# Optimization experiments

Measured on AMD Instinct MI355X. Metric: run time of the kernel, lower is better.

## Reference

```python
import jax, jax.numpy as jnp
import numpy as np
from jax.scipy.linalg import solve_triangular

REG = 1e-6  # reg_covar added to covariance diagonal
LOG2PI = float(np.log(2.0 * np.pi))
RESP_EPS = 10.0 * float(np.finfo(np.float32).eps)


def _log_gauss(X, means, covs):
    # X: [N,D], means: [K,D], covs: [K,D,D] -> per-sample per-component log N(x|mu_k, Sigma_k): [N,K]
    K, D = means.shape
    eye = jnp.eye(D, dtype=X.dtype)
    chol = jnp.linalg.cholesky(covs + REG * eye)                      # [K,D,D]
    diff = X[None, :, :] - means[:, None, :]                          # [K,N,D]
    sol = jax.vmap(lambda L, d: solve_triangular(L, d.T, lower=True))(chol, diff)  # [K,D,N]
    maha = jnp.sum(sol * sol, axis=1)                                 # [K,N]
    logdet = jnp.sum(jnp.log(jnp.diagonal(chol, axis1=1, axis2=2)), axis=1)  # [K] = 0.5*log|Sigma|
    return (-0.5 * (D * LOG2PI + maha) - logdet[:, None]).T           # [N,K]


def _em_step(X, weights, means, covs):
    N, D = X.shape
    # E-step: responsibilities via stable logsumexp
    lp = _log_gauss(X, means, covs) + jnp.log(weights)[None, :]       # [N,K]
    log_norm = jax.scipy.special.logsumexp(lp, axis=1)                # [N]
    resp = jnp.exp(lp - log_norm[:, None])                            # [N,K]
    # M-step (MLE)
    nk = resp.sum(axis=0) + RESP_EPS                                  # [K]
    new_w = nk / N
    new_means = (resp.T @ X) / nk[:, None]                            # [K,D]
    diff = X[None, :, :] - new_means[:, None, :]                      # [K,N,D]
    new_covs = jnp.einsum('kn,knd,kne->kde', resp.T, diff, diff) / nk[:, None, None]
    new_covs = new_covs + REG * jnp.eye(D, dtype=X.dtype)
    return new_w, new_means, new_covs


def reference(X, weights, means, covariances, n_iter):
    # Normalize provided weights (uniform init in the torch module)
    w0 = weights / jnp.sum(weights)

    def step(carry, _):
        w, m, c = carry
        return _em_step(X, w, m, c), None

    (w, m, c), _ = jax.lax.scan(step, (w0, means, covariances), xs=None, length=n_iter)
    # Final per-sample log-likelihood under the fitted mixture (lower bound)
    lp = _log_gauss(X, m, c) + jnp.log(w)[None, :]
    return jax.scipy.special.logsumexp(lp, axis=1)                    # [N]


def setup_inputs() -> dict:
    key = jax.random.key(0)
    kx, km = jax.random.split(key)
    N, D, K = 100000, 32, 16
    X = jax.random.normal(kx, (N, D), dtype=jnp.float32)
    weights = jnp.ones((K,), dtype=jnp.float32) / K
    means = jax.random.normal(km, (K, D), dtype=jnp.float32)
    covariances = jnp.tile(jnp.eye(D, dtype=jnp.float32)[None], (K, 1, 1))
    return {"X": X, "weights": weights, "means": means, "covariances": covariances, "n_iter": 5}
```

## Files before the change

kernel.cpp:

```cpp
#include <hip/hip_runtime.h>
#include <math.h>

#define REGC 1e-6f
#define LOG2PI 1.83787706640934534f
#define RESP_EPS 1.1920929e-6f

#define NPART_MAX 256
#define PART_K 1156
#define PART_BLK (16 * PART_K)
#define RS 16

typedef __attribute__((ext_vector_type(8))) short short8;
typedef __attribute__((ext_vector_type(4))) float f32x4;
typedef unsigned short ushort_t;
typedef unsigned int uint_t;

__device__ __forceinline__ ushort_t f2bf(float x) {
    uint_t u = __float_as_uint(x);
    uint_t r = (u + 0x7fffu + ((u >> 16) & 1u)) >> 16;
    return (ushort_t)r;
}
__device__ __forceinline__ float bf2f(ushort_t h) {
    return __uint_as_float(((uint_t)h) << 16);
}
__device__ __forceinline__ f32x4 shx4(f32x4 v, int m) {
    f32x4 r;
#pragma unroll
    for (int i = 0; i < 4; ++i) r[i] = __shfl_xor(v[i], m);
    return r;
}
__device__ __forceinline__ f32x4 sel4(bool s, f32x4 b, f32x4 a) {
    f32x4 r;
#pragma unroll
    for (int i = 0; i < 4; ++i) r[i] = s ? b[i] : a[i];
    return r;
}

__global__ void gmm_init(const float* __restrict__ w, const float* __restrict__ mu,
                         const float* __restrict__ cov, float* __restrict__ P0) {
    int t = blockIdx.x * 256 + threadIdx.x;
    if (t < 16) {
        float s = 0.f;
        for (int i = 0; i < 16; ++i) s += w[i];
        P0[t] = w[t] / s;
    } else if (t < 528) {
        P0[t] = mu[t - 16];
    } else if (t < 16912) {
        P0[t] = cov[t - 528];
    }
}

__global__ __launch_bounds__(256) void gmm_xsplit(const float* __restrict__ X,
                                                  ushort_t* __restrict__ Xh,
                                                  ushort_t* __restrict__ Xl,
                                                  ushort_t* __restrict__ XTH,
                                                  int N) {
    int chunk = blockIdx.x;
    int t = threadIdx.x;
    __shared__ float xsh[32][33];
    int s = t >> 3, q = t & 7;
    int n = chunk * 32 + s;
    float4 v = make_float4(0.f, 0.f, 0.f, 0.f);
    if (n < N) v = ((const float4*)(X + (size_t)n * 32))[q];
    float vv[4] = { v.x, v.y, v.z, v.w };
    xsh[s][q * 4 + 0] = v.x; xsh[s][q * 4 + 1] = v.y;
    xsh[s][q * 4 + 2] = v.z; xsh[s][q * 4 + 3] = v.w;
    if (n < N) {
        ushort_t h[4], l[4];
#pragma unroll
        for (int i = 0; i < 4; ++i) {
            h[i] = f2bf(vv[i]);
            l[i] = f2bf(vv[i] - bf2f(h[i]));
        }
        size_t o = (size_t)n * 32 + q * 4;
        uint2 hp = make_uint2((uint_t)h[0] | ((uint_t)h[1] << 16),
                              (uint_t)h[2] | ((uint_t)h[3] << 16));
        uint2 lp = make_uint2((uint_t)l[0] | ((uint_t)l[1] << 16),
                              (uint_t)l[2] | ((uint_t)l[3] << 16));
        *(uint2*)(Xh + o) = hp;
        *(uint2*)(Xl + o) = lp;
    }
    __syncthreads();
    int di = t >> 7;
    int lane = (t >> 1) & 63;
    int jj0 = (t & 1) * 4;
    int c = lane & 15, quad = lane >> 4;
    int d = di * 16 + c;
    ushort_t fh[4];
#pragma unroll
    for (int i = 0; i < 4; ++i) fh[i] = f2bf(xsh[quad * 8 + jj0 + i][d]);
    size_t fo = ((size_t)(chunk * 2 + di) * 64 + lane) * 8 + jj0;
    uint2 hp = make_uint2((uint_t)fh[0] | ((uint_t)fh[1] << 16),
                          (uint_t)fh[2] | ((uint_t)fh[3] << 16));
    *(uint2*)(XTH + fo) = hp;
}

__global__ __launch_bounds__(64) void gmm_prep(const float* __restrict__ P,
                                               ushort_t* __restrict__ Wh,
                                               ushort_t* __restrict__ Wl,
                                               float* __restrict__ Bv,
                                               float* __restrict__ Cc) {
    int k = blockIdx.x;
    int t = threadIdx.x;
    __shared__ float L[32][33];
    __shared__ float Ai[32][33];
    const float* cov = P + 528 + k * 1024;
    const float* mu  = P + 16 + k * 32;

#pragma unroll
    for (int rep = 0; rep < 16; ++rep) {
        int idx = rep * 64 + t;
        int i = idx >> 5, j = idx & 31;
        L[i][j] = cov[idx] + (i == j ? REGC : 0.f);
    }
    __syncthreads();

#pragma unroll
    for (int j = 0; j < 32; ++j) {
        float s = L[j][j];
#pragma unroll
        for (int p = 0; p < j; ++p) { float v = L[j][p]; s -= v * v; }
        float dj = sqrtf(s);
        if (t > j && t < 32) {
            float s2 = L[t][j];
#pragma unroll
            for (int p = 0; p < j; ++p) s2 -= L[t][p] * L[j][p];
            L[t][j] = s2 / dj;
        }
        if (t == j) L[j][j] = dj;
        __syncthreads();
    }

    if (t < 32) {
        float ai[32];
#pragma unroll
        for (int r = 0; r < 32; ++r) {
            float s = (r == t) ? 1.f : 0.f;
#pragma unroll
            for (int p = 0; p < r; ++p) s -= L[r][p] * ai[p];
            ai[r] = s / L[r][r];
        }
#pragma unroll
        for (int r = 0; r < 32; ++r) Ai[r][t] = ai[r];
    }
    __syncthreads();

#pragma unroll
    for (int rep = 0; rep < 16; ++rep) {
        int idx = rep * 64 + t;
        int i = idx >> 5, j = idx & 31;
        float v = Ai[i][j];
        ushort_t h = f2bf(v);
        Wh[(size_t)(k * 32 + i) * 32 + j] = h;
        Wl[(size_t)(k * 32 + i) * 32 + j] = f2bf(v - bf2f(h));
    }
    if (t < 32) {
        float s = 0.f;
#pragma unroll
        for (int j = 0; j < 32; ++j) s += Ai[t][j] * mu[j];
        Bv[k * 32 + t] = s;
    }
    float lv = (t < 32) ? logf(L[t & 31][t & 31]) : 0.f;
#pragma unroll
    for (int off = 1; off < 32; off <<= 1) lv += __shfl_xor(lv, off);
    if (t == 0) Cc[k] = logf(P[k]) - 0.5f * 32.0f * LOG2PI - lv;
}

__global__ __launch_bounds__(256, 2) void gmm_estep(const ushort_t* __restrict__ Xh,
                                                    const ushort_t* __restrict__ Xl,
                                                    const ushort_t* __restrict__ Wh,
                                                    const ushort_t* __restrict__ Wl,
                                                    const float* __restrict__ Bv,
                                                    const float* __restrict__ Cc,
                                                    float* __restrict__ resp,
                                                    float* __restrict__ out,
                                                    int N, int mode) {
    int t = threadIdx.x;
    int wave = t >> 6, lane = t & 63;
    int quad = lane >> 4, c = lane & 15;
    int wstart = (blockIdx.x * 4 + wave) * 32;
    if (wstart + 32 > N) wstart = (N >= 32) ? (N - 32) : 0;
    bool al4 = ((N & 3) == 0);

    size_t xo0 = (size_t)(wstart + c) * 32 + quad * 8;
    size_t xo1 = (size_t)(wstart + 16 + c) * 32 + quad * 8;
    short8 ah0 = *(const short8*)(Xh + xo0);
    short8 al0 = *(const short8*)(Xl + xo0);
    short8 ah1 = *(const short8*)(Xh + xo1);
    short8 al1 = *(const short8*)(Xl + xo1);

    f32x4 p0[2], p1[2], p2[2], p3[2], fin[2];

#pragma unroll
    for (int k = 0; k < 16; ++k) {
        size_t w0 = (size_t)(k * 32 + c) * 32 + quad * 8;
        size_t w1 = w0 + 512;
        short8 bh0 = *(const short8*)(Wh + w0);
        short8 bl0 = *(const short8*)(Wl + w0);
        short8 bh1 = *(const short8*)(Wh + w1);
        short8 bl1 = *(const short8*)(Wl + w1);
        float bv0 = Bv[k * 32 + c];
        float bv1 = Bv[k * 32 + 16 + c];
#pragma unroll
        for (int tt = 0; tt < 2; ++tt) {
            short8 ah = tt ? ah1 : ah0;
            short8 al = tt ? al1 : al0;
            f32x4 a0 = {0.f, 0.f, 0.f, 0.f};
            f32x4 a1 = {0.f, 0.f, 0.f, 0.f};
            a0 = __builtin_amdgcn_mfma_f32_16x16x32_bf16(ah, bh0, a0, 0, 0, 0);
            a0 = __builtin_amdgcn_mfma_f32_16x16x32_bf16(ah, bl0, a0, 0, 0, 0);
            a0 = __builtin_amdgcn_mfma_f32_16x16x32_bf16(al, bh0, a0, 0, 0, 0);
            a1 = __builtin_amdgcn_mfma_f32_16x16x32_bf16(ah, bh1, a1, 0, 0, 0);
            a1 = __builtin_amdgcn_mfma_f32_16x16x32_bf16(ah, bl1, a1, 0, 0, 0);
            a1 = __builtin_amdgcn_mfma_f32_16x16x32_bf16(al, bh1, a1, 0, 0, 0);
            f32x4 ms;
#pragma unroll
            for (int r = 0; r < 4; ++r) {
                float d0 = a0[r] - bv0;
                float d1 = a1[r] - bv1;
                ms[r] = fmaf(d0, d0, d1 * d1);
            }
            if ((k & 1) == 0) { p0[tt] = ms; }
            else {
                f32x4 a = p0[tt] + shx4(p0[tt], 1);
                f32x4 b = ms + shx4(ms, 1);
                f32x4 v = sel4((c & 1) != 0, b, a);
                if ((k & 2) == 0) { p1[tt] = v; }
                else {
                    a = p1[tt] + shx4(p1[tt], 2); b = v + shx4(v, 2); v = sel4((c & 2) != 0, b, a);
                    if ((k & 4) == 0) { p2[tt] = v; }
                    else {
                        a = p2[tt] + shx4(p2[tt], 4); b = v + shx4(v, 4); v = sel4((c & 4) != 0, b, a);
                        if ((k & 8) == 0) { p3[tt] = v; }
                        else {
                            a = p3[tt] + shx4(p3[tt], 8); b = v + shx4(v, 8);
                            fin[tt] = sel4((c & 8) != 0, b, a);
                        }
                    }
                }
            }
        }
    }

    float cc = Cc[c];
#pragma unroll
    for (int tt = 0; tt < 2; ++tt) {
        f32x4 lp;
#pragma unroll
        for (int r = 0; r < 4; ++r) lp[r] = cc - 0.5f * fin[tt][r];
        f32x4 mx = lp;
#pragma unroll
        for (int off = 1; off < 16; off <<= 1) {
            f32x4 s = shx4(mx, off);
#pragma unroll
            for (int r = 0; r < 4; ++r) mx[r] = fmaxf(mx[r], s[r]);
        }
        f32x4 e;
#pragma unroll
        for (int r = 0; r < 4; ++r) e[r] = __expf(lp[r] - mx[r]);
        f32x4 sm = e;
#pragma unroll
        for (int off = 1; off < 16; off <<= 1) sm = sm + shx4(sm, off);

        int nb = wstart + tt * 16 + quad * 4;
        if (mode) {
            if (c == 0) {
                f32x4 o;
#pragma unroll
                for (int r = 0; r < 4; ++r) o[r] = mx[r] + __logf(sm[r]);
                if (al4) *(f32x4*)(out + nb) = o;
                else { for (int r = 0; r < 4; ++r) out[nb + r] = o[r]; }
            }
        } else {
            f32x4 sv;
#pragma unroll
            for (int r = 0; r < 4; ++r) sv[r] = e[r] / sm[r];
            size_t off = (size_t)c * N + nb;
            if (al4) *(f32x4*)(resp + off) = sv;
            else { for (int r = 0; r < 4; ++r) resp[off + r] = sv[r]; }
        }
    }
}

__global__ __launch_bounds__(1024, 4) void gmm_moment(const ushort_t* __restrict__ XTH,
                                                      const float* __restrict__ resp,
                                                      float* __restrict__ part,
                                                      int N, int NC) {
    int t = threadIdx.x;
    int k = t >> 6;
    int lane = t & 63;
    int quad = lane >> 4, c = lane & 15;
    bool al4 = ((N & 3) == 0);

    f32x4 acc00 = {0.f,0.f,0.f,0.f}, acc01 = {0.f,0.f,0.f,0.f};
    f32x4 acc10 = {0.f,0.f,0.f,0.f}, acc11 = {0.f,0.f,0.f,0.f};
    float row0 = 0.f, row1 = 0.f, corner = 0.f;

#pragma unroll 1
    for (int chunk = blockIdx.x; chunk < NC; chunk += gridDim.x) {
        size_t fb = ((size_t)chunk * 2 * 64 + lane) * 8;
        short8 bh0 = *(const short8*)(XTH + fb);
        short8 bh1 = *(const short8*)(XTH + fb + 512);

        const float* rp = resp + (size_t)k * N + (size_t)chunk * 32 + quad * 8;
        float r[8];
        if (al4) {
            float4 ra = *(const float4*)rp;
            float4 rb = *(const float4*)(rp + 4);
            r[0]=ra.x; r[1]=ra.y; r[2]=ra.z; r[3]=ra.w;
            r[4]=rb.x; r[5]=rb.y; r[6]=rb.z; r[7]=rb.w;
        } else {
#pragma unroll
            for (int j = 0; j < 8; ++j) r[j] = rp[j];
        }
        corner += ((r[0]+r[1])+(r[2]+r[3])) + ((r[4]+r[5])+(r[6]+r[7]));

        short8 a0, a1;
#pragma unroll
        for (int jj = 0; jj < 8; ++jj) {
            float x0 = bf2f((ushort_t)bh0[jj]);
            float av0 = r[jj] * x0;
            a0[jj] = (short)f2bf(av0);
            row0 += av0;
            float x1 = bf2f((ushort_t)bh1[jj]);
            float av1 = r[jj] * x1;
            a1[jj] = (short)f2bf(av1);
            row1 += av1;
        }

        acc00 = __builtin_amdgcn_mfma_f32_16x16x32_bf16(a0, bh0, acc00, 0, 0, 0);
        acc01 = __builtin_amdgcn_mfma_f32_16x16x32_bf16(a0, bh1, acc01, 0, 0, 0);
        acc10 = __builtin_amdgcn_mfma_f32_16x16x32_bf16(a1, bh0, acc10, 0, 0, 0);
        acc11 = __builtin_amdgcn_mfma_f32_16x16x32_bf16(a1, bh1, acc11, 0, 0, 0);
    }

    row0 += __shfl_xor(row0, 16);  row0 += __shfl_xor(row0, 32);
    row1 += __shfl_xor(row1, 16);  row1 += __shfl_xor(row1, 32);
    corner += __shfl_xor(corner, 16);  corner += __shfl_xor(corner, 32);

    float* pb = part + ((size_t)blockIdx.x * 16 + k) * PART_K;
#pragma unroll
    for (int r = 0; r < 4; ++r) {
        pb[(quad * 4 + r) * 34 + c]            = acc00[r];
        pb[(quad * 4 + r) * 34 + 16 + c]       = acc01[r];
        pb[(16 + quad * 4 + r) * 34 + c]       = acc10[r];
        pb[(16 + quad * 4 + r) * 34 + 16 + c]  = acc11[r];
    }
    if (quad == 0) {
        pb[32 * 34 + c]      = row0;
        pb[32 * 34 + 16 + c] = row1;
    }
    if (lane == 0) pb[32 * 34 + 32] = corner;
}

__global__ __launch_bounds__(256) void gmm_reduce1(const float* __restrict__ part,
                                                   float* __restrict__ part2,
                                                   int npart) {
    int k = blockIdx.x, g = blockIdx.y;
    int nb = (npart + RS - 1) / RS;
    int b0 = g * nb;
    int b1 = b0 + nb; if (b1 > npart) b1 = npart;
    for (int idx = threadIdx.x; idx < PART_K; idx += 256) {
        float s = 0.f;
#pragma unroll 4
        for (int b = b0; b < b1; ++b)
            s += part[((size_t)b * 16 + k) * PART_K + idx];
        part2[((size_t)g * 16 + k) * PART_K + idx] = s;
    }
}

__global__ __launch_bounds__(256) void gmm_redfin_prep(const float* __restrict__ part2,
                                                       ushort_t* __restrict__ Wh,
                                                       ushort_t* __restrict__ Wl,
                                                       float* __restrict__ Bv,
                                                       float* __restrict__ Cc,
                                                       int N) {
    int k = blockIdx.x;
    int t = threadIdx.x;
    __shared__ float S[1156];
    __shared__ float L[32][33];
    __shared__ float Ai[32][33];

    for (int idx = t; idx < 1156; idx += 256) {
        float s = 0.f;
#pragma unroll
        for (int b = 0; b < RS; ++b)
            s += part2[((size_t)b * 16 + k) * PART_K + idx];
        S[idx] = s;
    }
    __syncthreads();
    float nk = S[32 * 34 + 32] + RESP_EPS;
    float inv = 1.f / nk;
    for (int idx = t; idx < 1024; idx += 256) {
        int i = idx >> 5, j = idx & 31;
        float mi = S[32 * 34 + i] * inv;
        float mj = S[32 * 34 + j] * inv;
        L[i][j] = S[i * 34 + j] * inv - mi * mj + ((i == j) ? 2.f * REGC : 0.f);
    }
    __syncthreads();

#pragma unroll
    for (int j = 0; j < 32; ++j) {
        if (t < 32) {
            float s = L[j][j];
#pragma unroll
            for (int p = 0; p < j; ++p) { float v = L[j][p]; s -= v * v; }
            float dj = sqrtf(s);
            if (t > j) {
                float s2 = L[t][j];
#pragma unroll
                for (int p = 0; p < j; ++p) s2 -= L[t][p] * L[j][p];
                L[t][j] = s2 / dj;
            }
            if (t == j) L[j][j] = dj;
        }
        __syncthreads();
    }

    if (t < 32) {
        float ai[32];
#pragma unroll
        for (int r = 0; r < 32; ++r) {
            float s = (r == t) ? 1.f : 0.f;
#pragma unroll
            for (int p = 0; p < r; ++p) s -= L[r][p] * ai[p];
            ai[r] = s / L[r][r];
        }
#pragma unroll
        for (int r = 0; r < 32; ++r) Ai[r][t] = ai[r];
    }
    __syncthreads();

#pragma unroll
    for (int rep = 0; rep < 4; ++rep) {
        int idx = rep * 256 + t;
        int i = idx >> 5, j = idx & 31;
        float v = Ai[i][j];
        ushort_t h = f2bf(v);
        Wh[(size_t)(k * 32 + i) * 32 + j] = h;
        Wl[(size_t)(k * 32 + i) * 32 + j] = f2bf(v - bf2f(h));
    }
    if (t < 32) {
        float s = 0.f;
#pragma unroll
        for (int j = 0; j < 32; ++j) s += Ai[t][j] * (S[32 * 34 + j] * inv);
        Bv[k * 32 + t] = s;
    }
    float lv = (t < 32) ? logf(L[t & 31][t & 31]) : 0.f;
#pragma unroll
    for (int off = 1; off < 32; off <<= 1) lv += __shfl_xor(lv, off);
    if (t == 0) Cc[k] = logf(nk / (float)N) - 0.5f * 32.0f * LOG2PI - lv;
}

extern "C" void kernel_launch(void* const* d_in, const int* in_sizes, int n_in,
                              void* d_out, int out_size, void* d_ws, size_t ws_size,
                              hipStream_t stream) {
    const float* X   = (const float*)d_in[0];
    const float* w   = (const float*)d_in[1];
    const float* mu  = (const float*)d_in[2];
    const float* cov = (const float*)d_in[3];
    const int NITER = 5;
    int N = in_sizes[0] / 32;
    int NC = (N + 31) / 32;

    float* ws = (float*)d_ws;
    float*    P0 = ws;
    float*    Bv = ws + 16912;
    float*    Cc = ws + 17424;
    ushort_t* Wh = (ushort_t*)(ws + 17440);
    ushort_t* Wl = (ushort_t*)(ws + 25632);
    ushort_t* Xh = (ushort_t*)(ws + 33824);
    ushort_t* Xl = (ushort_t*)(ws + 33824 + (size_t)16 * N);
    size_t xt0 = 33824 + (size_t)32 * N;
    size_t SZ  = (size_t)NC * 512;
    ushort_t* XTH = (ushort_t*)(ws + xt0);
    float*  resp = ws + xt0 + SZ;
    size_t p2base = xt0 + SZ + (size_t)16 * N;
    float*  part2 = ws + p2base;
    size_t pbase = p2base + (size_t)RS * 16 * PART_K;
    float*  part = ws + pbase;

    long long avail = (long long)(ws_size / 4) - (long long)pbase;
    int npart = (int)(avail / PART_BLK);
    if (npart > NPART_MAX) npart = NPART_MAX;
    if (npart < 1) npart = 1;

    float* out = (float*)d_out;

    int eblocks = ((N + 31) / 32 + 3) / 4;

    gmm_init<<<67, 256, 0, stream>>>(w, mu, cov, P0);
    gmm_xsplit<<<NC, 256, 0, stream>>>(X, Xh, Xl, XTH, N);
    gmm_prep<<<16, 64, 0, stream>>>(P0, Wh, Wl, Bv, Cc);

    for (int it = 0; it < NITER; ++it) {
        gmm_estep<<<eblocks, 256, 0, stream>>>(Xh, Xl, Wh, Wl, Bv, Cc, resp, out, N, 0);
        gmm_moment<<<npart, 1024, 0, stream>>>(XTH, resp, part, N, NC);
        dim3 r1(16, RS);
        gmm_reduce1<<<r1, 256, 0, stream>>>(part, part2, npart);
        gmm_redfin_prep<<<16, 256, 0, stream>>>(part2, Wh, Wl, Bv, Cc, N);
    }
    gmm_estep<<<eblocks, 256, 0, stream>>>(Xh, Xl, Wh, Wl, Bv, Cc, resp, out, N, 1);
}
```

Before: 478.1 us.

## Fuse E-step and moment accumulation into one kernel via shared-memory responsibilities

```diff
diff --git a/kernel.cpp b/kernel.cpp
--- a/kernel.cpp
+++ b/kernel.cpp
@@ -5,10 +5,7 @@
 #define LOG2PI 1.83787706640934534f
 #define RESP_EPS 1.1920929e-6f
 
-#define NPART_MAX 256
 #define PART_K 1156
-#define PART_BLK (16 * PART_K)
-#define RS 16
 
 typedef __attribute__((ext_vector_type(8))) short short8;
 typedef __attribute__((ext_vector_type(4))) float f32x4;
@@ -34,20 +31,6 @@
 #pragma unroll
     for (int i = 0; i < 4; ++i) r[i] = s ? b[i] : a[i];
     return r;
-}
-
-__global__ void gmm_init(const float* __restrict__ w, const float* __restrict__ mu,
-                         const float* __restrict__ cov, float* __restrict__ P0) {
-    int t = blockIdx.x * 256 + threadIdx.x;
-    if (t < 16) {
-        float s = 0.f;
-        for (int i = 0; i < 16; ++i) s += w[i];
-        P0[t] = w[t] / s;
-    } else if (t < 528) {
-        P0[t] = mu[t - 16];
-    } else if (t < 16912) {
-        P0[t] = cov[t - 528];
-    }
 }
 
 __global__ __launch_bounds__(256) void gmm_xsplit(const float* __restrict__ X,
@@ -73,12 +56,10 @@
             l[i] = f2bf(vv[i] - bf2f(h[i]));
         }
         size_t o = (size_t)n * 32 + q * 4;
-        uint2 hp = make_uint2((uint_t)h[0] | ((uint_t)h[1] << 16),
-                              (uint_t)h[2] | ((uint_t)h[3] << 16));
-        uint2 lp = make_uint2((uint_t)l[0] | ((uint_t)l[1] << 16),
-                              (uint_t)l[2] | ((uint_t)l[3] << 16));
-        *(uint2*)(Xh + o) = hp;
-        *(uint2*)(Xl + o) = lp;
+        *(uint2*)(Xh + o) = make_uint2((uint_t)h[0] | ((uint_t)h[1] << 16),
+                                       (uint_t)h[2] | ((uint_t)h[3] << 16));
+        *(uint2*)(Xl + o) = make_uint2((uint_t)l[0] | ((uint_t)l[1] << 16),
+                                       (uint_t)l[2] | ((uint_t)l[3] << 16));
     }
     __syncthreads();
     int di = t >> 7;
@@ -90,31 +71,30 @@
 #pragma unroll
     for (int i = 0; i < 4; ++i) fh[i] = f2bf(xsh[quad * 8 + jj0 + i][d]);
     size_t fo = ((size_t)(chunk * 2 + di) * 64 + lane) * 8 + jj0;
-    uint2 hp = make_uint2((uint_t)fh[0] | ((uint_t)fh[1] << 16),
-                          (uint_t)fh[2] | ((uint_t)fh[3] << 16));
-    *(uint2*)(XTH + fo) = hp;
-}
-
-__global__ __launch_bounds__(64) void gmm_prep(const float* __restrict__ P,
-                                               ushort_t* __restrict__ Wh,
-                                               ushort_t* __restrict__ Wl,
-                                               float* __restrict__ Bv,
-                                               float* __restrict__ Cc) {
+    *(uint2*)(XTH + fo) = make_uint2((uint_t)fh[0] | ((uint_t)fh[1] << 16),
+                                     (uint_t)fh[2] | ((uint_t)fh[3] << 16));
+}
+
+__global__ __launch_bounds__(64) void gmm_prep0(const float* __restrict__ w,
+                                                const float* __restrict__ mu,
+                                                const float* __restrict__ cov,
+                                                ushort_t* __restrict__ Wh,
+                                                ushort_t* __restrict__ Wl,
+                                                float* __restrict__ Bv,
+                                                float* __restrict__ Cc) {
     int k = blockIdx.x;
     int t = threadIdx.x;
     __shared__ float L[32][33];
     __shared__ float Ai[32][33];
-    const float* cov = P + 528 + k * 1024;
-    const float* mu  = P + 16 + k * 32;
-
+    const float* cv = cov + (size_t)k * 1024;
+    const float* muk = mu + (size_t)k * 32;
 #pragma unroll
     for (int rep = 0; rep < 16; ++rep) {
         int idx = rep * 64 + t;
         int i = idx >> 5, j = idx & 31;
-        L[i][j] = cov[idx] + (i == j ? REGC : 0.f);
-    }
-    __syncthreads();
-
+        L[i][j] = cv[idx] + (i == j ? REGC : 0.f);
+    }
+    __syncthreads();
 #pragma unroll
     for (int j = 0; j < 32; ++j) {
         float s = L[j][j];
@@ -130,7 +110,6 @@
         if (t == j) L[j][j] = dj;
         __syncthreads();
     }
-
     if (t < 32) {
         float ai[32];
 #pragma unroll
@@ -144,7 +123,6 @@
         for (int r = 0; r < 32; ++r) Ai[r][t] = ai[r];
     }
     __syncthreads();
-
 #pragma unroll
     for (int rep = 0; rep < 16; ++rep) {
         int idx = rep * 64 + t;
@@ -157,24 +135,259 @@
     if (t < 32) {
         float s = 0.f;
 #pragma unroll
-        for (int j = 0; j < 32; ++j) s += Ai[t][j] * mu[j];
+        for (int j = 0; j < 32; ++j) s += Ai[t][j] * muk[j];
         Bv[k * 32 + t] = s;
     }
+    float wsum = 0.f;
+#pragma unroll
+    for (int i = 0; i < 16; ++i) wsum += w[i];
     float lv = (t < 32) ? logf(L[t & 31][t & 31]) : 0.f;
 #pragma unroll
     for (int off = 1; off < 32; off <<= 1) lv += __shfl_xor(lv, off);
-    if (t == 0) Cc[k] = logf(P[k]) - 0.5f * 32.0f * LOG2PI - lv;
-}
-
-__global__ __launch_bounds__(256, 2) void gmm_estep(const ushort_t* __restrict__ Xh,
-                                                    const ushort_t* __restrict__ Xl,
-                                                    const ushort_t* __restrict__ Wh,
-                                                    const ushort_t* __restrict__ Wl,
-                                                    const float* __restrict__ Bv,
-                                                    const float* __restrict__ Cc,
-                                                    float* __restrict__ resp,
-                                                    float* __restrict__ out,
-                                                    int N, int mode) {
+    if (t == 0) Cc[k] = logf(w[k] / wsum) - 0.5f * 32.0f * LOG2PI - lv;
+}
+
+__global__ __launch_bounds__(1024) __attribute__((amdgpu_waves_per_eu(4, 4)))
+void gmm_emstep(const ushort_t* __restrict__ Xh, const ushort_t* __restrict__ Xl,
+                const ushort_t* __restrict__ XTH,
+                const ushort_t* __restrict__ Wh, const ushort_t* __restrict__ Wl,
+                const float* __restrict__ Bv, const float* __restrict__ Cc,
+                float* __restrict__ part, int N) {
+    __shared__ float rsh[16][516];
+    int t = threadIdx.x;
+    int wave = t >> 6, lane = t & 63;
+    int quad = lane >> 4, c = lane & 15;
+
+    int wstart0 = (int)blockIdx.x * 512 + wave * 32;
+    bool dup = (wstart0 + 32 > N);
+    int wst = dup ? ((N >= 32) ? N - 32 : 0) : wstart0;
+
+    size_t xo0 = (size_t)(wst + c) * 32 + quad * 8;
+    size_t xo1 = (size_t)(wst + 16 + c) * 32 + quad * 8;
+    short8 ah0 = *(const short8*)(Xh + xo0);
+    short8 al0 = *(const short8*)(Xl + xo0);
+    short8 ah1 = *(const short8*)(Xh + xo1);
+    short8 al1 = *(const short8*)(Xl + xo1);
+
+    {
+        f32x4 p0[2], p1[2], p2[2], p3[2], fin[2];
+#pragma unroll
+        for (int k = 0; k < 16; ++k) {
+            size_t w0 = (size_t)(k * 32 + c) * 32 + quad * 8;
+            size_t w1 = w0 + 512;
+            short8 bh0 = *(const short8*)(Wh + w0);
+            short8 bl0 = *(const short8*)(Wl + w0);
+            short8 bh1 = *(const short8*)(Wh + w1);
+            short8 bl1 = *(const short8*)(Wl + w1);
+            float bv0 = Bv[k * 32 + c];
+            float bv1 = Bv[k * 32 + 16 + c];
+#pragma unroll
+            for (int tt = 0; tt < 2; ++tt) {
+                short8 ah = tt ? ah1 : ah0;
+                short8 al = tt ? al1 : al0;
+                f32x4 a0 = {0.f, 0.f, 0.f, 0.f};
+                f32x4 a1 = {0.f, 0.f, 0.f, 0.f};
+                a0 = __builtin_amdgcn_mfma_f32_16x16x32_bf16(ah, bh0, a0, 0, 0, 0);
+                a0 = __builtin_amdgcn_mfma_f32_16x16x32_bf16(ah, bl0, a0, 0, 0, 0);
+                a0 = __builtin_amdgcn_mfma_f32_16x16x32_bf16(al, bh0, a0, 0, 0, 0);
+                a1 = __builtin_amdgcn_mfma_f32_16x16x32_bf16(ah, bh1, a1, 0, 0, 0);
+                a1 = __builtin_amdgcn_mfma_f32_16x16x32_bf16(ah, bl1, a1, 0, 0, 0);
+                a1 = __builtin_amdgcn_mfma_f32_16x16x32_bf16(al, bh1, a1, 0, 0, 0);
+                f32x4 ms;
+#pragma unroll
+                for (int r = 0; r < 4; ++r) {
+                    float d0 = a0[r] - bv0;
+                    float d1 = a1[r] - bv1;
+                    ms[r] = fmaf(d0, d0, d1 * d1);
+                }
+                if ((k & 1) == 0) { p0[tt] = ms; }
+                else {
+                    f32x4 a = p0[tt] + shx4(p0[tt], 1);
+                    f32x4 b = ms + shx4(ms, 1);
+                    f32x4 v = sel4((c & 1) != 0, b, a);
+                    if ((k & 2) == 0) { p1[tt] = v; }
+                    else {
+                        a = p1[tt] + shx4(p1[tt], 2); b = v + shx4(v, 2); v = sel4((c & 2) != 0, b, a);
+                        if ((k & 4) == 0) { p2[tt] = v; }
+                        else {
+                            a = p2[tt] + shx4(p2[tt], 4); b = v + shx4(v, 4); v = sel4((c & 4) != 0, b, a);
+                            if ((k & 8) == 0) { p3[tt] = v; }
+                            else {
+                                a = p3[tt] + shx4(p3[tt], 8); b = v + shx4(v, 8);
+                                fin[tt] = sel4((c & 8) != 0, b, a);
+                            }
+                        }
+                    }
+                }
+            }
+        }
+        float ccv = Cc[c];
+#pragma unroll
+        for (int tt = 0; tt < 2; ++tt) {
+            f32x4 lp;
+#pragma unroll
+            for (int r = 0; r < 4; ++r) lp[r] = ccv - 0.5f * fin[tt][r];
+            f32x4 mx = lp;
+#pragma unroll
+            for (int off = 1; off < 16; off <<= 1) {
+                f32x4 s = shx4(mx, off);
+#pragma unroll
+                for (int r = 0; r < 4; ++r) mx[r] = fmaxf(mx[r], s[r]);
+            }
+            f32x4 e;
+#pragma unroll
+            for (int r = 0; r < 4; ++r) e[r] = __expf(lp[r] - mx[r]);
+            f32x4 sm = e;
+#pragma unroll
+            for (int off = 1; off < 16; off <<= 1) sm = sm + shx4(sm, off);
+            f32x4 sv;
+#pragma unroll
+            for (int r = 0; r < 4; ++r) sv[r] = dup ? 0.f : e[r] / sm[r];
+            *(f32x4*)&rsh[c][wave * 32 + tt * 16 + quad * 4] = sv;
+        }
+    }
+    __syncthreads();
+
+    {
+        int k = wave;
+        f32x4 m00 = {0.f,0.f,0.f,0.f}, m01 = {0.f,0.f,0.f,0.f};
+        f32x4 m10 = {0.f,0.f,0.f,0.f}, m11 = {0.f,0.f,0.f,0.f};
+        float row0 = 0.f, row1 = 0.f, corner = 0.f;
+#pragma unroll 4
+        for (int ch = 0; ch < 16; ++ch) {
+            size_t fb = (((size_t)((int)blockIdx.x * 16 + ch)) * 128 + lane) * 8;
+            short8 bh0 = *(const short8*)(XTH + fb);
+            short8 bh1 = *(const short8*)(XTH + fb + 512);
+            float r8[8];
+#pragma unroll
+            for (int jj = 0; jj < 8; ++jj) r8[jj] = rsh[k][ch * 32 + quad * 8 + jj];
+            corner += ((r8[0]+r8[1])+(r8[2]+r8[3])) + ((r8[4]+r8[5])+(r8[6]+r8[7]));
+            short8 a0, a1;
+#pragma unroll
+            for (int jj = 0; jj < 8; ++jj) {
+                float x0 = bf2f((ushort_t)bh0[jj]);
+                float av0 = r8[jj] * x0;
+                a0[jj] = (short)f2bf(av0);
+                row0 += av0;
+                float x1 = bf2f((ushort_t)bh1[jj]);
+                float av1 = r8[jj] * x1;
+                a1[jj] = (short)f2bf(av1);
+                row1 += av1;
+            }
+            m00 = __builtin_amdgcn_mfma_f32_16x16x32_bf16(a0, bh0, m00, 0, 0, 0);
+            m01 = __builtin_amdgcn_mfma_f32_16x16x32_bf16(a0, bh1, m01, 0, 0, 0);
+            m10 = __builtin_amdgcn_mfma_f32_16x16x32_bf16(a1, bh0, m10, 0, 0, 0);
+            m11 = __builtin_amdgcn_mfma_f32_16x16x32_bf16(a1, bh1, m11, 0, 0, 0);
+        }
+        row0 += __shfl_xor(row0, 16);  row0 += __shfl_xor(row0, 32);
+        row1 += __shfl_xor(row1, 16);  row1 += __shfl_xor(row1, 32);
+        corner += __shfl_xor(corner, 16);  corner += __shfl_xor(corner, 32);
+
+        float* pb = part + ((size_t)blockIdx.x * 16 + k) * PART_K;
+#pragma unroll
+        for (int r = 0; r < 4; ++r) {
+            pb[(quad * 4 + r) * 34 + c]           = m00[r];
+            pb[(quad * 4 + r) * 34 + 16 + c]      = m01[r];
+            pb[(16 + quad * 4 + r) * 34 + c]      = m10[r];
+            pb[(16 + quad * 4 + r) * 34 + 16 + c] = m11[r];
+        }
+        if (quad == 0) {
+            pb[32 * 34 + c]      = row0;
+            pb[32 * 34 + 16 + c] = row1;
+        }
+        if (lane == 0) pb[32 * 34 + 32] = corner;
+    }
+}
+
+__global__ __launch_bounds__(1024) void gmm_redfin_prep(const float* __restrict__ part,
+                                                        ushort_t* __restrict__ Wh,
+                                                        ushort_t* __restrict__ Wl,
+                                                        float* __restrict__ Bv,
+                                                        float* __restrict__ Cc,
+                                                        int N, int npart) {
+    int k = blockIdx.x;
+    int t = threadIdx.x;
+    __shared__ float S[1156];
+    __shared__ float L[1056];
+    __shared__ float Ai[1056];
+    __shared__ float mean[32];
+
+    for (int idx = t; idx < 1121; idx += 1024) {
+        float s = 0.f;
+#pragma unroll 4
+        for (int b = 0; b < npart; ++b)
+            s += part[((size_t)b * 16 + k) * PART_K + idx];
+        S[idx] = s;
+    }
+    __syncthreads();
+    float nk = S[32 * 34 + 32] + RESP_EPS;
+    float inv = 1.f / nk;
+    {
+        int i = t >> 5, j = t & 31;
+        float mi = S[32 * 34 + i] * inv;
+        float mj = S[32 * 34 + j] * inv;
+        L[i * 33 + j] = S[i * 34 + j] * inv - mi * mj + ((i == j) ? 2.f * REGC : 0.f);
+    }
+    if (t < 32) mean[t] = S[32 * 34 + t] * inv;
+    __syncthreads();
+
+#pragma unroll
+    for (int j = 0; j < 32; ++j) {
+        if (t < 32) {
+            float s = L[j * 33 + j];
+#pragma unroll
+            for (int p = 0; p < j; ++p) { float v = L[j * 33 + p]; s -= v * v; }
+            float dj = sqrtf(s);
+            if (t > j) {
+                float s2 = L[t * 33 + j];
+#pragma unroll
+                for (int p = 0; p < j; ++p) s2 -= L[t * 33 + p] * L[j * 33 + p];
+                L[t * 33 + j] = s2 / dj;
+            }
+            if (t == j) L[j * 33 + j] = dj;
+        }
+        __syncthreads();
+    }
+    if (t < 32) {
+        float ai[32];
+#pragma unroll
+        for (int r = 0; r < 32; ++r) {
+            float s = (r == t) ? 1.f : 0.f;
+#pragma unroll
+            for (int p = 0; p < r; ++p) s -= L[r * 33 + p] * ai[p];
+            ai[r] = s / L[r * 33 + r];
+        }
+#pragma unroll
+        for (int r = 0; r < 32; ++r) Ai[r * 33 + t] = ai[r];
+    }
+    __syncthreads();
+    {
+        int i = t >> 5, j = t & 31;
+        float v = Ai[i * 33 + j];
+        ushort_t h = f2bf(v);
+        Wh[(size_t)(k * 32 + i) * 32 + j] = h;
+        Wl[(size_t)(k * 32 + i) * 32 + j] = f2bf(v - bf2f(h));
+    }
+    if (t < 32) {
+        float s = 0.f;
+#pragma unroll
+        for (int j = 0; j < 32; ++j) s += Ai[t * 33 + j] * mean[j];
+        Bv[k * 32 + t] = s;
+    }
+    float lv = (t < 32) ? logf(L[(t & 31) * 33 + (t & 31)]) : 0.f;
+#pragma unroll
+    for (int off = 1; off < 32; off <<= 1) lv += __shfl_xor(lv, off);
+    if (t == 0) Cc[k] = logf(nk / (float)N) - 0.5f * 32.0f * LOG2PI - lv;
+}
+
+__global__ __launch_bounds__(256, 2) void gmm_estep_fin(const ushort_t* __restrict__ Xh,
+                                                        const ushort_t* __restrict__ Xl,
+                                                        const ushort_t* __restrict__ Wh,
+                                                        const ushort_t* __restrict__ Wl,
+                                                        const float* __restrict__ Bv,
+                                                        const float* __restrict__ Cc,
+                                                        float* __restrict__ out,
+                                                        int N) {
     int t = threadIdx.x;
     int wave = t >> 6, lane = t & 63;
     int quad = lane >> 4, c = lane & 15;
@@ -190,7 +403,6 @@
     short8 al1 = *(const short8*)(Xl + xo1);
 
     f32x4 p0[2], p1[2], p2[2], p3[2], fin[2];
-
 #pragma unroll
     for (int k = 0; k < 16; ++k) {
         size_t w0 = (size_t)(k * 32 + c) * 32 + quad * 8;
@@ -241,13 +453,12 @@
             }
         }
     }
-
-    float cc = Cc[c];
+    float ccv = Cc[c];
 #pragma unroll
     for (int tt = 0; tt < 2; ++tt) {
         f32x4 lp;
 #pragma unroll
-        for (int r = 0; r < 4; ++r) lp[r] = cc - 0.5f * fin[tt][r];
+        for (int r = 0; r < 4; ++r) lp[r] = ccv - 0.5f * fin[tt][r];
         f32x4 mx = lp;
 #pragma unroll
         for (int off = 1; off < 16; off <<= 1) {
@@ -261,195 +472,15 @@
         f32x4 sm = e;
 #pragma unroll
         for (int off = 1; off < 16; off <<= 1) sm = sm + shx4(sm, off);
-
-        int nb = wstart + tt * 16 + quad * 4;
-        if (mode) {
-            if (c == 0) {
-                f32x4 o;
-#pragma unroll
-                for (int r = 0; r < 4; ++r) o[r] = mx[r] + __logf(sm[r]);
-                if (al4) *(f32x4*)(out + nb) = o;
-                else { for (int r = 0; r < 4; ++r) out[nb + r] = o[r]; }
-            }
-        } else {
-            f32x4 sv;
-#pragma unroll
-            for (int r = 0; r < 4; ++r) sv[r] = e[r] / sm[r];
-            size_t off = (size_t)c * N + nb;
-            if (al4) *(f32x4*)(resp + off) = sv;
-            else { for (int r = 0; r < 4; ++r) resp[off + r] = sv[r]; }
-        }
-    }
-}
-
-__global__ __launch_bounds__(1024, 4) void gmm_moment(const ushort_t* __restrict__ XTH,
-                                                      const float* __restrict__ resp,
-                                                      float* __restrict__ part,
-                                                      int N, int NC) {
-    int t = threadIdx.x;
-    int k = t >> 6;
-    int lane = t & 63;
-    int quad = lane >> 4, c = lane & 15;
-    bool al4 = ((N & 3) == 0);
-
-    f32x4 acc00 = {0.f,0.f,0.f,0.f}, acc01 = {0.f,0.f,0.f,0.f};
-    f32x4 acc10 = {0.f,0.f,0.f,0.f}, acc11 = {0.f,0.f,0.f,0.f};
-    float row0 = 0.f, row1 = 0.f, corner = 0.f;
-
-#pragma unroll 1
-    for (int chunk = blockIdx.x; chunk < NC; chunk += gridDim.x) {
-        size_t fb = ((size_t)chunk * 2 * 64 + lane) * 8;
-        short8 bh0 = *(const short8*)(XTH + fb);
-        short8 bh1 = *(const short8*)(XTH + fb + 512);
-
-        const float* rp = resp + (size_t)k * N + (size_t)chunk * 32 + quad * 8;
-        float r[8];
-        if (al4) {
-            float4 ra = *(const float4*)rp;
-            float4 rb = *(const float4*)(rp + 4);
-            r[0]=ra.x; r[1]=ra.y; r[2]=ra.z; r[3]=ra.w;
-            r[4]=rb.x; r[5]=rb.y; r[6]=rb.z; r[7]=rb.w;
-        } else {
-#pragma unroll
-            for (int j = 0; j < 8; ++j) r[j] = rp[j];
-        }
-        corner += ((r[0]+r[1])+(r[2]+r[3])) + ((r[4]+r[5])+(r[6]+r[7]));
-
-        short8 a0, a1;
-#pragma unroll
-        for (int jj = 0; jj < 8; ++jj) {
-            float x0 = bf2f((ushort_t)bh0[jj]);
-            float av0 = r[jj] * x0;
-            a0[jj] = (short)f2bf(av0);
-            row0 += av0;
-            float x1 = bf2f((ushort_t)bh1[jj]);
-            float av1 = r[jj] * x1;
-            a1[jj] = (short)f2bf(av1);
-            row1 += av1;
-        }
-
-        acc00 = __builtin_amdgcn_mfma_f32_16x16x32_bf16(a0, bh0, acc00, 0, 0, 0);
-        acc01 = __builtin_amdgcn_mfma_f32_16x16x32_bf16(a0, bh1, acc01, 0, 0, 0);
-        acc10 = __builtin_amdgcn_mfma_f32_16x16x32_bf16(a1, bh0, acc10, 0, 0, 0);
-        acc11 = __builtin_amdgcn_mfma_f32_16x16x32_bf16(a1, bh1, acc11, 0, 0, 0);
-    }
-
-    row0 += __shfl_xor(row0, 16);  row0 += __shfl_xor(row0, 32);
-    row1 += __shfl_xor(row1, 16);  row1 += __shfl_xor(row1, 32);
-    corner += __shfl_xor(corner, 16);  corner += __shfl_xor(corner, 32);
-
-    float* pb = part + ((size_t)blockIdx.x * 16 + k) * PART_K;
-#pragma unroll
-    for (int r = 0; r < 4; ++r) {
-        pb[(quad * 4 + r) * 34 + c]            = acc00[r];
-        pb[(quad * 4 + r) * 34 + 16 + c]       = acc01[r];
-        pb[(16 + quad * 4 + r) * 34 + c]       = acc10[r];
-        pb[(16 + quad * 4 + r) * 34 + 16 + c]  = acc11[r];
-    }
-    if (quad == 0) {
-        pb[32 * 34 + c]      = row0;
-        pb[32 * 34 + 16 + c] = row1;
-    }
-    if (lane == 0) pb[32 * 34 + 32] = corner;
-}
-
-__global__ __launch_bounds__(256) void gmm_reduce1(const float* __restrict__ part,
-                                                   float* __restrict__ part2,
-                                                   int npart) {
-    int k = blockIdx.x, g = blockIdx.y;
-    int nb = (npart + RS - 1) / RS;
-    int b0 = g * nb;
-    int b1 = b0 + nb; if (b1 > npart) b1 = npart;
-    for (int idx = threadIdx.x; idx < PART_K; idx += 256) {
-        float s = 0.f;
-#pragma unroll 4
-        for (int b = b0; b < b1; ++b)
-            s += part[((size_t)b * 16 + k) * PART_K + idx];
-        part2[((size_t)g * 16 + k) * PART_K + idx] = s;
-    }
-}
-
-__global__ __launch_bounds__(256) void gmm_redfin_prep(const float* __restrict__ part2,
-                                                       ushort_t* __restrict__ Wh,
-                                                       ushort_t* __restrict__ Wl,
-                                                       float* __restrict__ Bv,
-                                                       float* __restrict__ Cc,
-                                                       int N) {
-    int k = blockIdx.x;
-    int t = threadIdx.x;
-    __shared__ float S[1156];
-    __shared__ float L[32][33];
-    __shared__ float Ai[32][33];
-
-    for (int idx = t; idx < 1156; idx += 256) {
-        float s = 0.f;
-#pragma unroll
-        for (int b = 0; b < RS; ++b)
-            s += part2[((size_t)b * 16 + k) * PART_K + idx];
-        S[idx] = s;
-    }
-    __syncthreads();
-    float nk = S[32 * 34 + 32] + RESP_EPS;
-    float inv = 1.f / nk;
-    for (int idx = t; idx < 1024; idx += 256) {
-        int i = idx >> 5, j = idx & 31;
-        float mi = S[32 * 34 + i] * inv;
-        float mj = S[32 * 34 + j] * inv;
-        L[i][j] = S[i * 34 + j] * inv - mi * mj + ((i == j) ? 2.f * REGC : 0.f);
-    }
-    __syncthreads();
-
-#pragma unroll
-    for (int j = 0; j < 32; ++j) {
-        if (t < 32) {
-            float s = L[j][j];
-#pragma unroll
-            for (int p = 0; p < j; ++p) { float v = L[j][p]; s -= v * v; }
-            float dj = sqrtf(s);
-            if (t > j) {
-                float s2 = L[t][j];
-#pragma unroll
-                for (int p = 0; p < j; ++p) s2 -= L[t][p] * L[j][p];
-                L[t][j] = s2 / dj;
-            }
-            if (t == j) L[j][j] = dj;
-        }
-        __syncthreads();
-    }
-
-    if (t < 32) {
-        float ai[32];
-#pragma unroll
-        for (int r = 0; r < 32; ++r) {
-            float s = (r == t) ? 1.f : 0.f;
-#pragma unroll
-            for (int p = 0; p < r; ++p) s -= L[r][p] * ai[p];
-            ai[r] = s / L[r][r];
-        }
-#pragma unroll
-        for (int r = 0; r < 32; ++r) Ai[r][t] = ai[r];
-    }
-    __syncthreads();
-
-#pragma unroll
-    for (int rep = 0; rep < 4; ++rep) {
-        int idx = rep * 256 + t;
-        int i = idx >> 5, j = idx & 31;
-        float v = Ai[i][j];
-        ushort_t h = f2bf(v);
-        Wh[(size_t)(k * 32 + i) * 32 + j] = h;
-        Wl[(size_t)(k * 32 + i) * 32 + j] = f2bf(v - bf2f(h));
-    }
-    if (t < 32) {
-        float s = 0.f;
-#pragma unroll
-        for (int j = 0; j < 32; ++j) s += Ai[t][j] * (S[32 * 34 + j] * inv);
-        Bv[k * 32 + t] = s;
-    }
-    float lv = (t < 32) ? logf(L[t & 31][t & 31]) : 0.f;
-#pragma unroll
-    for (int off = 1; off < 32; off <<= 1) lv += __shfl_xor(lv, off);
-    if (t == 0) Cc[k] = logf(nk / (float)N) - 0.5f * 32.0f * LOG2PI - lv;
+        if (c == 0) {
+            int nb = wstart + tt * 16 + quad * 4;
+            f32x4 o;
+#pragma unroll
+            for (int r = 0; r < 4; ++r) o[r] = mx[r] + __logf(sm[r]);
+            if (al4) *(f32x4*)(out + nb) = o;
+            else { for (int r = 0; r < 4; ++r) out[nb + r] = o[r]; }
+        }
+    }
 }
 
 extern "C" void kernel_launch(void* const* d_in, const int* in_sizes, int n_in,
@@ -461,44 +492,31 @@
     const float* cov = (const float*)d_in[3];
     const int NITER = 5;
     int N = in_sizes[0] / 32;
-    int NC = (N + 31) / 32;
+    int NB = (N + 511) / 512;
+    int NCB = NB * 16;
 
     float* ws = (float*)d_ws;
-    float*    P0 = ws;
-    float*    Bv = ws + 16912;
-    float*    Cc = ws + 17424;
-    ushort_t* Wh = (ushort_t*)(ws + 17440);
-    ushort_t* Wl = (ushort_t*)(ws + 25632);
-    ushort_t* Xh = (ushort_t*)(ws + 33824);
-    ushort_t* Xl = (ushort_t*)(ws + 33824 + (size_t)16 * N);
-    size_t xt0 = 33824 + (size_t)32 * N;
-    size_t SZ  = (size_t)NC * 512;
+    float*    Bv = ws;
+    float*    Cc = ws + 512;
+    ushort_t* Wh = (ushort_t*)(ws + 528);
+    ushort_t* Wl = (ushort_t*)(ws + 8720);
+    ushort_t* Xh = (ushort_t*)(ws + 16912);
+    ushort_t* Xl = (ushort_t*)(ws + 16912 + (size_t)16 * N);
+    size_t xt0 = 16912 + (size_t)32 * N;
+    size_t SZ  = (size_t)NCB * 512;
     ushort_t* XTH = (ushort_t*)(ws + xt0);
-    float*  resp = ws + xt0 + SZ;
-    size_t p2base = xt0 + SZ + (size_t)16 * N;
-    float*  part2 = ws + p2base;
-    size_t pbase = p2base + (size_t)RS * 16 * PART_K;
-    float*  part = ws + pbase;
-
-    long long avail = (long long)(ws_size / 4) - (long long)pbase;
-    int npart = (int)(avail / PART_BLK);
-    if (npart > NPART_MAX) npart = NPART_MAX;
-    if (npart < 1) npart = 1;
+    float*  part = ws + xt0 + SZ;
 
     float* out = (float*)d_out;
 
     int eblocks = ((N + 31) / 32 + 3) / 4;
 
-    gmm_init<<<67, 256, 0, stream>>>(w, mu, cov, P0);
-    gmm_xsplit<<<NC, 256, 0, stream>>>(X, Xh, Xl, XTH, N);
-    gmm_prep<<<16, 64, 0, stream>>>(P0, Wh, Wl, Bv, Cc);
+    gmm_xsplit<<<NCB, 256, 0, stream>>>(X, Xh, Xl, XTH, N);
+    gmm_prep0<<<16, 64, 0, stream>>>(w, mu, cov, Wh, Wl, Bv, Cc);
 
     for (int it = 0; it < NITER; ++it) {
-        gmm_estep<<<eblocks, 256, 0, stream>>>(Xh, Xl, Wh, Wl, Bv, Cc, resp, out, N, 0);
-        gmm_moment<<<npart, 1024, 0, stream>>>(XTH, resp, part, N, NC);
-        dim3 r1(16, RS);
-        gmm_reduce1<<<r1, 256, 0, stream>>>(part, part2, npart);
-        gmm_redfin_prep<<<16, 256, 0, stream>>>(part2, Wh, Wl, Bv, Cc, N);
-    }
-    gmm_estep<<<eblocks, 256, 0, stream>>>(Xh, Xl, Wh, Wl, Bv, Cc, resp, out, N, 1);
-}
+        gmm_emstep<<<NB, 1024, 0, stream>>>(Xh, Xl, XTH, Wh, Wl, Bv, Cc, part, N);
+        gmm_redfin_prep<<<16, 1024, 0, stream>>>(part, Wh, Wl, Bv, Cc, N, NB);
+    }
+    gmm_estep_fin<<<eblocks, 256, 0, stream>>>(Xh, Xl, Wh, Wl, Bv, Cc, out, N);
+}
```

Result: slower. 577.5 us (+20.8%).
